# Kernel optimization log

Measured on AMD Instinct MI355X. Metric: run time of the kernel, lower is better.

## Reference

```python
import jax, jax.numpy as jnp
import numpy as np

B, S, D = 1, 2048, 1024
H, HD = 16, 64          # attention heads, head dim
DFF = 4096              # ffn hidden
IH, ID = 4, 64          # indexer heads / dim ('baseline' strategy)
TOP_K = 64
ROPE_BASE = 10000.0
LN_EPS = 1e-5


def setup_inputs() -> dict:
    key = jax.random.key(0)
    ks = jax.random.split(key, 12)
    g = lambda k, shape: (jax.random.normal(k, shape, dtype=jnp.float32) * 0.02)
    return {
        "x": jax.random.normal(ks[0], (B, S, D), dtype=jnp.float32),
        "w_qkv": g(ks[1], (D, 3 * D)),
        "w_o": g(ks[2], (D, D)),
        "ffn_w1": g(ks[3], (D, DFF)),
        "ffn_b1": jnp.zeros((DFF,), jnp.float32),
        "ffn_w2": g(ks[4], (DFF, D)),
        "ffn_b2": jnp.zeros((D,), jnp.float32),
        "ln1_g": jnp.ones((D,), jnp.float32),
        "ln1_b": jnp.zeros((D,), jnp.float32),
        "ln2_g": jnp.ones((D,), jnp.float32),
        "ln2_b": jnp.zeros((D,), jnp.float32),
        "idx_wq": g(ks[5], (D, IH * ID)),
        "idx_wk": g(ks[6], (D, ID)),
        "idx_ww": g(ks[7], (D, IH)),
    }


def _layernorm(x, g, b):
    m = jnp.mean(x, axis=-1, keepdims=True)
    v = jnp.var(x, axis=-1, keepdims=True)
    return (x - m) * jax.lax.rsqrt(v + LN_EPS) * g + b


def _rope(x):  # x: [B,S,H,HD], torchtune interleaved-pair convention
    half = HD // 2
    theta = 1.0 / (ROPE_BASE ** (jnp.arange(0, HD, 2, dtype=jnp.float32) / HD))  # [half]
    ang = jnp.arange(S, dtype=jnp.float32)[:, None] * theta                      # [S,half]
    cos = jnp.cos(ang)[None, :, None, :]
    sin = jnp.sin(ang)[None, :, None, :]
    xp = x.reshape(*x.shape[:-1], half, 2)
    x0, x1 = xp[..., 0], xp[..., 1]
    out = jnp.stack([x0 * cos - x1 * sin, x1 * cos + x0 * sin], axis=-1)
    return out.reshape(x.shape)


def reference(x, w_qkv, w_o, ffn_w1, ffn_b1, ffn_w2, ffn_b2,
              ln1_g, ln1_b, ln2_g, ln2_b, idx_wq, idx_wk, idx_ww):
    norm_x = _layernorm(x, ln1_g, ln1_b)

    qkv = norm_x @ w_qkv                              # [B,S,3D]
    q, k, v = jnp.split(qkv, 3, axis=-1)
    q = _rope(q.reshape(B, S, H, HD))
    k = _rope(k.reshape(B, S, H, HD))
    v = v.reshape(B, S, H, HD)

    # Lightning-style indexer: I[t,s] = sum_h w[t,h] * relu(q_i[t,h] . k_i[s])
    qi = (norm_x @ idx_wq).reshape(B, S, IH, ID)      # [B,S,IH,ID]
    ki = norm_x @ idx_wk                              # [B,S,ID]
    wi = norm_x @ idx_ww                              # [B,S,IH]
    qk = jnp.einsum("bthd,bsd->bths", qi, ki)         # [B,S,IH,S]
    index_scores = jnp.einsum("bth,bths->bts", wi, jax.nn.relu(qk))  # [B,S,S]

    # causal top-k token selection -> boolean mask
    causal = jnp.tril(jnp.ones((S, S), dtype=bool))
    masked_scores = jnp.where(causal, index_scores, -jnp.inf)
    _, topk_idx = jax.lax.top_k(masked_scores, TOP_K)  # [B,S,K]
    b_ix = jnp.arange(B)[:, None, None]
    q_ix = jnp.arange(S)[None, :, None]
    mask = jnp.zeros((B, S, S), dtype=bool).at[b_ix, q_ix, topk_idx].set(True)
    mask = mask & causal                               # [B,S,S]

    # masked SDPA
    logits = jnp.einsum("bqhd,bkhd->bhqk", q, k) / np.sqrt(HD)
    logits = jnp.where(mask[:, None, :, :], logits, -jnp.inf)
    attn = jax.nn.softmax(logits, axis=-1)
    attn_out = jnp.einsum("bhqk,bkhd->bqhd", attn, v).reshape(B, S, D)
    x = x + attn_out @ w_o

    h = _layernorm(x, ln2_g, ln2_b)
    ffn = jax.nn.gelu(h @ ffn_w1 + ffn_b1, approximate=False) @ ffn_w2 + ffn_b2
    return x + ffn
```

## Files before the change

kernel.cpp:

```cpp
#include <hip/hip_runtime.h>
#include <math.h>

#define S_LEN 2048
#define D_MODEL 1024
#define NHEAD 16
#define HDIM 64
#define DFF 4096
#define IH 4
#define IDM 64
#define TOPK 64
#define NIDX 336

typedef float f32x4 __attribute__((ext_vector_type(4)));
typedef short bf16x8 __attribute__((ext_vector_type(8)));

__device__ __forceinline__ unsigned short f2bf(float f) {
    unsigned u = __builtin_bit_cast(unsigned, f);
    u += 0x7fff + ((u >> 16) & 1);
    return (unsigned short)(u >> 16);
}
__device__ __forceinline__ float bf2f(unsigned short us) {
    return __builtin_bit_cast(float, (unsigned)us << 16);
}

__device__ __forceinline__ float gelu_exact(float v) {
    return 0.5f * v * (1.f + erff(v * 0.70710678118654752f));
}

__device__ __forceinline__ void gl_lds16(const void* g, void* l) {
    __builtin_amdgcn_global_load_lds(
        (const __attribute__((address_space(1))) void*)g,
        (__attribute__((address_space(3))) void*)l, 16, 0, 0);
}

__global__ __launch_bounds__(256) void ln_kernel(const float* __restrict__ x,
    const float* __restrict__ g, const float* __restrict__ b,
    float* __restrict__ outf, unsigned short* __restrict__ outb)
{
    int row = blockIdx.x, tid = threadIdx.x;
    const float4 v = *(const float4*)(x + (size_t)row * D_MODEL + tid * 4);
    float s = v.x + v.y + v.z + v.w;
    float ss = v.x * v.x + v.y * v.y + v.z * v.z + v.w * v.w;
    int lane = tid & 63, wv = tid >> 6;
    for (int o = 32; o; o >>= 1) { s += __shfl_xor(s, o); ss += __shfl_xor(ss, o); }
    __shared__ float rs[4], rss[4];
    if (lane == 0) { rs[wv] = s; rss[wv] = ss; }
    __syncthreads();
    float S = rs[0] + rs[1] + rs[2] + rs[3];
    float SS = rss[0] + rss[1] + rss[2] + rss[3];
    float mean = S * (1.f / D_MODEL);
    float var = SS * (1.f / D_MODEL) - mean * mean;
    float r = rsqrtf(var + 1e-5f);
    float4 gv = *(const float4*)(g + tid * 4);
    float4 bv = *(const float4*)(b + tid * 4);
    float4 o4;
    o4.x = (v.x - mean) * r * gv.x + bv.x;
    o4.y = (v.y - mean) * r * gv.y + bv.y;
    o4.z = (v.z - mean) * r * gv.z + bv.z;
    o4.w = (v.w - mean) * r * gv.w + bv.w;
    if (outf) *(float4*)(outf + (size_t)row * D_MODEL + tid * 4) = o4;
    if (outb) {
        ushort4 u4 = { f2bf(o4.x), f2bf(o4.y), f2bf(o4.z), f2bf(o4.w) };
        *(ushort4*)(outb + (size_t)row * D_MODEL + tid * 4) = u4;
    }
}

__global__ __launch_bounds__(256) void wtrans_kernel(const float* __restrict__ in,
    unsigned short* __restrict__ out, int K, int N)
{
    __shared__ float t[32][33];
    int k0 = blockIdx.y * 32, n0 = blockIdx.x * 32;
    int tid = threadIdx.x;
    int r = tid >> 5, c = tid & 31;
#pragma unroll
    for (int p = 0; p < 4; ++p)
        t[r + p * 8][c] = in[(size_t)(k0 + r + p * 8) * N + n0 + c];
    __syncthreads();
#pragma unroll
    for (int p = 0; p < 4; ++p)
        out[(size_t)(n0 + r + p * 8) * K + k0 + c] = f2bf(t[c][r + p * 8]);
}

__global__ __launch_bounds__(256) void wpack_kernel(const float* __restrict__ wq,
    const float* __restrict__ wk, const float* __restrict__ ww, float* __restrict__ Wc)
{
    int idx = blockIdx.x * 256 + threadIdx.x;
    if (idx >= D_MODEL * NIDX) return;
    int r = idx / NIDX, c = idx % NIDX;
    float v = 0.f;
    if (c < 256) v = wq[r * 256 + c];
    else if (c < 320) v = wk[r * 64 + (c - 256)];
    else if (c < 324) v = ww[r * 4 + (c - 320)];
    Wc[idx] = v;
}

__global__ __launch_bounds__(256) void gemm_bf16_n64(
    const unsigned short* __restrict__ A, const unsigned short* __restrict__ Bt,
    float* __restrict__ C, unsigned short* __restrict__ Cb,
    const float* __restrict__ bias, const float* __restrict__ R,
    int M, int N, int K, int act,
    float* __restrict__ P, int kchunk)
{
    __shared__ __attribute__((aligned(16))) unsigned short As[3][128 * 32];
    __shared__ __attribute__((aligned(16))) unsigned short Bs[3][64 * 32];
    int tid = threadIdx.x;
    int bm = blockIdx.y * 128, bn = blockIdx.x * 64;
    int wid = tid >> 6, lane = tid & 63;
    int wm = wid * 32;
    const unsigned short* Ab = A + (size_t)bm * K;
    const unsigned short* Bb = Bt + (size_t)bn * K;
    f32x4 acc[2][4];
#pragma unroll
    for (int i = 0; i < 2; ++i)
#pragma unroll
        for (int j = 0; j < 4; ++j)
            acc[i][j] = (f32x4){0.f, 0.f, 0.f, 0.f};

    int kbeg = blockIdx.z * kchunk;
    int NT = kchunk >> 5;
    int fr = lane & 15, fk = (lane >> 4) * 8;
    int e0 = tid * 8;
    int r0 = e0 >> 5, c0 = e0 & 31;

    auto STAGE = [&](int kt, int buf) {
        int k0 = kbeg + kt * 32;
        gl_lds16(Ab + (size_t)r0 * K + k0 + c0, &As[buf][e0]);
        gl_lds16(Ab + (size_t)(r0 + 64) * K + k0 + c0, &As[buf][e0 + 2048]);
        gl_lds16(Bb + (size_t)r0 * K + k0 + c0, &Bs[buf][e0]);
    };
    auto COMPUTE = [&](int buf) {
        bf16x8 af[2], bfv[4];
#pragma unroll
        for (int mi = 0; mi < 2; ++mi)
            af[mi] = *(const bf16x8*)&As[buf][(wm + mi * 16 + fr) * 32 + fk];
#pragma unroll
        for (int ni = 0; ni < 4; ++ni)
            bfv[ni] = *(const bf16x8*)&Bs[buf][(ni * 16 + fr) * 32 + fk];
#pragma unroll
        for (int mi = 0; mi < 2; ++mi)
#pragma unroll
            for (int ni = 0; ni < 4; ++ni)
                acc[mi][ni] = __builtin_amdgcn_mfma_f32_16x16x32_bf16(
                    af[mi], bfv[ni], acc[mi][ni], 0, 0, 0);
    };

    STAGE(0, 0);
    STAGE(1, 1);
    asm volatile("s_waitcnt vmcnt(3)" ::: "memory");
    __builtin_amdgcn_s_barrier();

    int kt = 0;
    for (; kt < NT - 2; ++kt) {
        STAGE(kt + 2, (kt + 2) % 3);
        COMPUTE(kt % 3);
        asm volatile("s_waitcnt vmcnt(3)" ::: "memory");
        __builtin_amdgcn_s_barrier();
    }
    COMPUTE((NT - 2) % 3);
    asm volatile("s_waitcnt vmcnt(0)" ::: "memory");
    __builtin_amdgcn_s_barrier();
    COMPUTE((NT - 1) % 3);

    int cl = lane & 15, rh = (lane >> 4) * 4;
    if (P) {
        float* Pz = P + (size_t)blockIdx.z * M * N;
#pragma unroll
        for (int mi = 0; mi < 2; ++mi)
#pragma unroll
            for (int ni = 0; ni < 4; ++ni) {
                int col = bn + ni * 16 + cl;
#pragma unroll
                for (int r = 0; r < 4; ++r) {
                    int row = bm + wm + mi * 16 + rh + r;
                    Pz[(size_t)row * N + col] = acc[mi][ni][r];
                }
            }
        return;
    }
#pragma unroll
    for (int mi = 0; mi < 2; ++mi) {
#pragma unroll
        for (int ni = 0; ni < 4; ++ni) {
            int col = bn + ni * 16 + cl;
            float bv = bias ? bias[col] : 0.f;
#pragma unroll
            for (int r = 0; r < 4; ++r) {
                int row = bm + wm + mi * 16 + rh + r;
                float v = acc[mi][ni][r] + bv;
                if (act) v = gelu_exact(v);
                size_t off = (size_t)row * N + col;
                if (R) v += R[off];
                if (C) C[off] = v;
                if (Cb) Cb[off] = f2bf(v);
            }
        }
    }
}

__global__ __launch_bounds__(256) void kreduce_kernel(const float* __restrict__ P,
    int nslice, float* __restrict__ C, const float* __restrict__ bias,
    const float* __restrict__ R, int M, int N)
{
    size_t total4 = (size_t)M * N / 4;
    size_t stride = (size_t)gridDim.x * 256;
    for (size_t i4 = blockIdx.x * 256 + threadIdx.x; i4 < total4; i4 += stride) {
        size_t off = i4 * 4;
        float4 v = *(const float4*)(P + off);
        for (int z = 1; z < nslice; ++z) {
            float4 p = *(const float4*)(P + (size_t)z * M * N + off);
            v.x += p.x; v.y += p.y; v.z += p.z; v.w += p.w;
        }
        if (bias) {
            float4 b4 = *(const float4*)(bias + (off % N));
            v.x += b4.x; v.y += b4.y; v.z += b4.z; v.w += b4.w;
        }
        if (R) {
            float4 r4 = *(const float4*)(R + off);
            v.x += r4.x; v.y += r4.y; v.z += r4.z; v.w += r4.w;
        }
        *(float4*)(C + off) = v;
    }
}

__global__ __launch_bounds__(256) void gemm64(const float* __restrict__ A,
    const float* __restrict__ B, float* __restrict__ C,
    int M, int N, int K,
    float* __restrict__ P, int kchunk)
{
    __shared__ float As[16][68];
    __shared__ float Bs[16][68];
    int tid = threadIdx.x;
    int bm = blockIdx.y, bn = blockIdx.x;
    int tx = tid & 15, ty = tid >> 4;
    int arow = tid >> 2;
    int acol = (tid & 3) << 2;
    int brow = tid >> 4;
    int bcol = (tid & 15) << 2;
    const float* Abase = A + (size_t)(bm * 64 + arow) * K + acol;
    float c[4][4] = {};
    int kbeg = blockIdx.z * kchunk;
    int kend = kbeg + kchunk;
    for (int k0 = kbeg; k0 < kend; k0 += 16) {
        float4 av = *(const float4*)(Abase + k0);
        As[acol + 0][arow] = av.x;
        As[acol + 1][arow] = av.y;
        As[acol + 2][arow] = av.z;
        As[acol + 3][arow] = av.w;
        int gcol = bn * 64 + bcol;
        const float* Bb = B + (size_t)(k0 + brow) * N;
        float4 bv;
        if (gcol + 3 < N) {
            bv = *(const float4*)(Bb + gcol);
        } else {
            bv.x = (gcol + 0 < N) ? Bb[gcol + 0] : 0.f;
            bv.y = (gcol + 1 < N) ? Bb[gcol + 1] : 0.f;
            bv.z = (gcol + 2 < N) ? Bb[gcol + 2] : 0.f;
            bv.w = (gcol + 3 < N) ? Bb[gcol + 3] : 0.f;
        }
        *(float4*)&Bs[brow][bcol] = bv;
        __syncthreads();
#pragma unroll
        for (int kk = 0; kk < 16; ++kk) {
            float4 a4 = *(const float4*)&As[kk][ty * 4];
            float4 b4 = *(const float4*)&Bs[kk][tx * 4];
            float av4[4] = { a4.x, a4.y, a4.z, a4.w };
            float bv4[4] = { b4.x, b4.y, b4.z, b4.w };
#pragma unroll
            for (int i = 0; i < 4; ++i)
#pragma unroll
                for (int j = 0; j < 4; ++j)
                    c[i][j] += av4[i] * bv4[j];
        }
        __syncthreads();
    }
    float* Out = P ? (P + (size_t)blockIdx.z * M * N) : C;
#pragma unroll
    for (int i = 0; i < 4; ++i) {
        int row = bm * 64 + ty * 4 + i;
#pragma unroll
        for (int j = 0; j < 4; ++j) {
            int col = bn * 64 + tx * 4 + j;
            if (col < N)
                Out[(size_t)row * N + col] = c[i][j];
        }
    }
}

__global__ __launch_bounds__(256) void rope_table_kernel(float* __restrict__ ct, float* __restrict__ st)
{
    int g = blockIdx.x * 256 + threadIdx.x;
    int t = g >> 5, i = g & 31;
    float theta = powf(10000.f, -(float)i / 32.f);
    float ang = (float)t * theta;
    ct[g] = cosf(ang);
    st[g] = sinf(ang);
}

__global__ __launch_bounds__(512) void rope_pack_kernel(
    const unsigned short* __restrict__ qkvb,
    const float* __restrict__ ct, const float* __restrict__ st,
    unsigned short* __restrict__ Qb, unsigned short* __restrict__ Kb,
    unsigned short* __restrict__ Vb)
{
    int t = blockIdx.x, tid = threadIdx.x;
    int h = tid >> 5, i = tid & 31;
    float c = ct[t * 32 + i], s = st[t * 32 + i];
    const unsigned short* base = qkvb + (size_t)t * (3 * D_MODEL);
    ushort2 q2 = *(const ushort2*)(base + h * HDIM + 2 * i);
    float q0 = bf2f(q2.x), q1 = bf2f(q2.y);
    ushort2 qo = { f2bf(q0 * c - q1 * s), f2bf(q1 * c + q0 * s) };
    *(ushort2*)(Qb + (size_t)t * D_MODEL + h * HDIM + 2 * i) = qo;
    ushort2 k2 = *(const ushort2*)(base + D_MODEL + h * HDIM + 2 * i);
    float k0 = bf2f(k2.x), k1 = bf2f(k2.y);
    ushort2 ko = { f2bf(k0 * c - k1 * s), f2bf(k1 * c + k0 * s) };
    *(ushort2*)(Kb + ((size_t)h * S_LEN + t) * HDIM + 2 * i) = ko;
    ushort2 v2 = *(const ushort2*)(base + 2 * D_MODEL + 2 * tid);
    int vh = tid >> 5, vd = (2 * tid) & 63;
    *(ushort2*)(Vb + ((size_t)vh * S_LEN + t) * HDIM + vd) = v2;
}

__global__ __launch_bounds__(256) void scores_kernel(const float* __restrict__ QIW,
    float* __restrict__ scores)
{
    int t0 = blockIdx.y * 64, s0 = blockIdx.x * 64;
    if (s0 > t0 + 63) return;
    __shared__ float qit[64][68];
    __shared__ float kit[64][68];
    __shared__ float wis[64][4];
    int tid = threadIdx.x;
    int tx = tid & 15, ty = tid >> 4;
    int lr = tid & 63;
    int cseg = tid >> 6;
    if (tid < 64) {
        float4 w4 = *(const float4*)(QIW + (size_t)(t0 + tid) * NIDX + 320);
        wis[tid][0] = w4.x; wis[tid][1] = w4.y; wis[tid][2] = w4.z; wis[tid][3] = w4.w;
    }
    float acc[4][4] = {};
#pragma unroll
    for (int h = 0; h < 4; ++h) {
        __syncthreads();
        const float* qrow = QIW + (size_t)(t0 + lr) * NIDX + h * 64 + cseg * 16;
        const float* krow = QIW + (size_t)(s0 + lr) * NIDX + 256 + cseg * 16;
#pragma unroll
        for (int q4 = 0; q4 < 4; ++q4) {
            int d = cseg * 16 + q4 * 4;
            float4 v = *(const float4*)(qrow + q4 * 4);
            qit[d + 0][lr] = v.x; qit[d + 1][lr] = v.y;
            qit[d + 2][lr] = v.z; qit[d + 3][lr] = v.w;
            if (h == 0) {
                float4 u = *(const float4*)(krow + q4 * 4);
                kit[d + 0][lr] = u.x; kit[d + 1][lr] = u.y;
                kit[d + 2][lr] = u.z; kit[d + 3][lr] = u.w;
            }
        }
        __syncthreads();
        float dot[4][4] = {};
#pragma unroll 8
        for (int d = 0; d < 64; ++d) {
            float4 a4 = *(const float4*)&qit[d][ty * 4];
            float4 b4 = *(const float4*)&kit[d][tx * 4];
            float av[4] = { a4.x, a4.y, a4.z, a4.w };
            float bv[4] = { b4.x, b4.y, b4.z, b4.w };
#pragma unroll
            for (int i = 0; i < 4; ++i)
#pragma unroll
                for (int j = 0; j < 4; ++j)
                    dot[i][j] += av[i] * bv[j];
        }
#pragma unroll
        for (int i = 0; i < 4; ++i) {
            float w = wis[ty * 4 + i][h];
#pragma unroll
            for (int j = 0; j < 4; ++j)
                acc[i][j] += w * fmaxf(dot[i][j], 0.f);
        }
    }
#pragma unroll
    for (int i = 0; i < 4; ++i) {
        float4 o4 = { acc[i][0], acc[i][1], acc[i][2], acc[i][3] };
        *(float4*)&scores[(size_t)(t0 + ty * 4 + i) * S_LEN + s0 + tx * 4] = o4;
    }
}

__global__ __launch_bounds__(256) void topk_kernel(const float* __restrict__ scores,
    int* __restrict__ topidx, int* __restrict__ topcnt)
{
    int t = blockIdx.x, tid = threadIdx.x;
    int n = t + 1;
    if (n <= TOPK) {
        if (tid < n) topidx[t * TOPK + tid] = tid;
        if (tid == 0) topcnt[t] = n;
        return;
    }
    __shared__ unsigned sc[S_LEN];
    __shared__ unsigned hist[256];
    __shared__ int selbin_s;
    __shared__ int cnt_out;
    __shared__ unsigned wsum[4];
    for (int j = tid; j < n; j += 256) {
        unsigned u = __builtin_bit_cast(unsigned, scores[(size_t)t * S_LEN + j]);
        sc[j] = (u & 0x80000000u) ? ~u : (u | 0x80000000u);
    }
    if (tid == 0) cnt_out = 0;
    int lane = tid & 63, wv = tid >> 6;
    unsigned prefix = 0;
    int kk = TOPK;
#pragma unroll
    for (int round = 0; round < 4; ++round) {
        int shift_pref = 32 - 8 * round;
        int shift_bin = 24 - 8 * round;
        hist[tid] = 0;
        __syncthreads();
        for (int j = tid; j < n; j += 256) {
            unsigned v = sc[j];
            if ((((unsigned long long)(v ^ prefix)) >> shift_pref) == 0)
                atomicAdd(&hist[(v >> shift_bin) & 0xff], 1u);
        }
        __syncthreads();
        if (wv == 0) {
            unsigned h0 = hist[4 * lane], h1 = hist[4 * lane + 1];
            unsigned h2 = hist[4 * lane + 2], h3 = hist[4 * lane + 3];
            unsigned s3 = h3, s2 = h2 + s3, s1 = h1 + s2, s0 = h0 + s1;
            unsigned acc = s0;
            for (int off = 1; off < 64; off <<= 1) {
                unsigned o = __shfl_down(acc, off);
                if (lane + off < 64) acc += o;
            }
            unsigned above = acc - s0;
            hist[4 * lane]     = s0 + above;
            hist[4 * lane + 1] = s1 + above;
            hist[4 * lane + 2] = s2 + above;
            hist[4 * lane + 3] = s3 + above;
        }
        __syncthreads();
        {
            unsigned sufb = hist[tid];
            unsigned sufn = (tid < 255) ? hist[tid + 1] : 0u;
            if (sufb >= (unsigned)kk && sufn < (unsigned)kk)
                selbin_s = tid;
        }
        __syncthreads();
        int b = selbin_s;
        unsigned above = (b < 255) ? hist[b + 1] : 0u;
        kk -= (int)above;
        prefix |= ((unsigned)b) << shift_bin;
        __syncthreads();
    }
    unsigned T = prefix;
    int chunk = (n + 255) >> 8;
    int jb = tid * chunk;
    int je = jb + chunk; if (je > n) je = n;
    int ties = 0;
    for (int j = jb; j < je; ++j) {
        unsigned v = sc[j];
        if (v > T) { int o = atomicAdd(&cnt_out, 1); topidx[t * TOPK + o] = j; }
        else if (v == T) ++ties;
    }
    unsigned inc = (unsigned)ties;
    for (int off = 1; off < 64; off <<= 1) {
        unsigned o = __shfl_up(inc, off);
        if (lane >= off) inc += o;
    }
    if (lane == 63) wsum[wv] = inc;
    __syncthreads();
    unsigned woff = 0;
    for (int w = 0; w < wv; ++w) woff += wsum[w];
    int rank = (int)(woff + inc) - ties;
    for (int j = jb; j < je && rank < kk; ++j) {
        if (sc[j] == T) {
            int o = atomicAdd(&cnt_out, 1);
            topidx[t * TOPK + o] = j;
            ++rank;
        }
    }
    if (tid == 0) topcnt[t] = TOPK;
}

__global__ __launch_bounds__(256) void attn_kernel(
    const unsigned short* __restrict__ Qb, const unsigned short* __restrict__ Kb,
    const unsigned short* __restrict__ Vb,
    const int* __restrict__ topidx, const int* __restrict__ topcnt,
    unsigned short* __restrict__ out)
{
    int t = blockIdx.x, tid = threadIdx.x;
    __shared__ int sel[TOPK];
    if (tid < TOPK) sel[tid] = topidx[t * TOPK + tid];
    __syncthreads();
    int cnt = topcnt[t];
    int lane = tid & 63, wv = tid >> 6;
    int h = blockIdx.y * 4 + wv;
    int klo = lane >> 3, oct = lane & 7;
    int rows[8];
    bool valid[8];
#pragma unroll
    for (int kg = 0; kg < 8; ++kg) {
        int k = kg * 8 + klo;
        valid[kg] = (k < cnt);
        rows[kg] = sel[valid[kg] ? k : 0];
    }
    bf16x8 q8 = *(const bf16x8*)(Qb + (size_t)t * D_MODEL + h * HDIM + oct * 8);
    float qf[8];
#pragma unroll
    for (int e = 0; e < 8; ++e) qf[e] = bf2f((unsigned short)q8[e]);

    const unsigned short* kbase = Kb + (size_t)h * S_LEN * HDIM + oct * 8;
    float p[8];
#pragma unroll
    for (int kg = 0; kg < 8; ++kg) {
        bf16x8 k8 = *(const bf16x8*)(kbase + (size_t)rows[kg] * HDIM);
        float d = 0.f;
#pragma unroll
        for (int e = 0; e < 8; ++e)
            d += bf2f((unsigned short)k8[e]) * qf[e];
        d += __shfl_xor(d, 1);
        d += __shfl_xor(d, 2);
        d += __shfl_xor(d, 4);
        p[kg] = valid[kg] ? d * 0.125f : -INFINITY;
    }
    float m = p[0];
#pragma unroll
    for (int kg = 1; kg < 8; ++kg) m = fmaxf(m, p[kg]);
    m = fmaxf(m, __shfl_xor(m, 8));
    m = fmaxf(m, __shfl_xor(m, 16));
    m = fmaxf(m, __shfl_xor(m, 32));
    float sum = 0.f;
#pragma unroll
    for (int kg = 0; kg < 8; ++kg) { p[kg] = __expf(p[kg] - m); sum += p[kg]; }
    sum += __shfl_xor(sum, 8);
    sum += __shfl_xor(sum, 16);
    sum += __shfl_xor(sum, 32);
    float rs = 1.f / sum;
    const unsigned short* vbase = Vb + (size_t)h * S_LEN * HDIM + oct * 8;
    float facc[8] = {};
#pragma unroll
    for (int kg = 0; kg < 8; ++kg) {
        bf16x8 v8 = *(const bf16x8*)(vbase + (size_t)rows[kg] * HDIM);
        float pw = p[kg] * rs;
#pragma unroll
        for (int e = 0; e < 8; ++e)
            facc[e] += pw * bf2f((unsigned short)v8[e]);
    }
#pragma unroll
    for (int e = 0; e < 8; ++e) {
        facc[e] += __shfl_xor(facc[e], 8);
        facc[e] += __shfl_xor(facc[e], 16);
        facc[e] += __shfl_xor(facc[e], 32);
    }
    if (klo == 0) {
        ushort4 o0 = { f2bf(facc[0]), f2bf(facc[1]), f2bf(facc[2]), f2bf(facc[3]) };
        ushort4 o1 = { f2bf(facc[4]), f2bf(facc[5]), f2bf(facc[6]), f2bf(facc[7]) };
        *(ushort4*)(out + (size_t)t * D_MODEL + h * HDIM + oct * 8) = o0;
        *(ushort4*)(out + (size_t)t * D_MODEL + h * HDIM + oct * 8 + 4) = o1;
    }
}

extern "C" void kernel_launch(void* const* d_in, const int* in_sizes, int n_in,
                              void* d_out, int out_size, void* d_ws, size_t ws_size,
                              hipStream_t stream)
{
    const float* x      = (const float*)d_in[0];
    const float* w_qkv  = (const float*)d_in[1];
    const float* w_o    = (const float*)d_in[2];
    const float* ffn_w1 = (const float*)d_in[3];
    const float* ffn_b1 = (const float*)d_in[4];
    const float* ffn_w2 = (const float*)d_in[5];
    const float* ffn_b2 = (const float*)d_in[6];
    const float* ln1_g  = (const float*)d_in[7];
    const float* ln1_b  = (const float*)d_in[8];
    const float* ln2_g  = (const float*)d_in[9];
    const float* ln2_b  = (const float*)d_in[10];
    const float* idx_wq = (const float*)d_in[11];
    const float* idx_wk = (const float*)d_in[12];
    const float* idx_ww = (const float*)d_in[13];
    float* outp = (float*)d_out;

    const size_t MB = 1ull << 20;
    char* ws = (char*)d_ws;
    float*          normx    = (float*)(ws + 0);
    unsigned short* attno_bf = (unsigned short*)(ws + 0);
    float*          Pf2      = (float*)(ws + 0);
    unsigned short* normx_bf = (unsigned short*)(ws + 8 * MB);
    unsigned short* h2_bf    = normx_bf;
    unsigned short* qkv_bf   = (unsigned short*)(ws + 12 * MB);
    int*            topidx   = (int*)(ws + 12 * MB);
    int*            topcnt   = (int*)(ws + 12 * MB + 512 * 1024);
    unsigned short* wqkv_t   = (unsigned short*)(ws + 24 * MB);
    unsigned short* wo_t     = (unsigned short*)(ws + 30 * MB);
    unsigned short* w1_t     = (unsigned short*)(ws + 32 * MB);
    unsigned short* w2_t     = (unsigned short*)(ws + 40 * MB);
    unsigned short* Qb       = (unsigned short*)(ws + 48 * MB);
    unsigned short* Kb       = (unsigned short*)(ws + 52 * MB);
    unsigned short* Vb       = (unsigned short*)(ws + 56 * MB);
    float*          ctab     = (float*)(ws + 60 * MB);
    float*          stab     = (float*)(ws + 60 * MB + 256 * 1024);
    float*          P_idx    = (float*)(ws + 60 * MB);
    float*          scoresb  = (float*)(ws + 60 * MB);
    float*          Pwo      = (float*)(ws + 60 * MB);
    unsigned short* ffn1_bf  = (unsigned short*)(ws + 60 * MB);
    float*          QIW      = (float*)(ws + 76 * MB);
    float*          Wc       = (float*)(ws + 79 * MB);

    dim3 blk256(256);
    auto g64n = [](int N, int M) { return dim3(N / 64, M / 128); };

    ln_kernel<<<S_LEN, blk256, 0, stream>>>(x, ln1_g, ln1_b, normx, normx_bf);
    rope_table_kernel<<<(S_LEN * 32) / 256, blk256, 0, stream>>>(ctab, stab);
    wtrans_kernel<<<dim3(3 * D_MODEL / 32, D_MODEL / 32), blk256, 0, stream>>>(w_qkv, wqkv_t, D_MODEL, 3 * D_MODEL);
    wtrans_kernel<<<dim3(D_MODEL / 32, D_MODEL / 32), blk256, 0, stream>>>(w_o, wo_t, D_MODEL, D_MODEL);
    wtrans_kernel<<<dim3(DFF / 32, D_MODEL / 32), blk256, 0, stream>>>(ffn_w1, w1_t, D_MODEL, DFF);
    wtrans_kernel<<<dim3(D_MODEL / 32, DFF / 32), blk256, 0, stream>>>(ffn_w2, w2_t, DFF, D_MODEL);
    wpack_kernel<<<(D_MODEL * NIDX + 255) / 256, blk256, 0, stream>>>(idx_wq, idx_wk, idx_ww, Wc);
    gemm_bf16_n64<<<g64n(3 * D_MODEL, S_LEN), blk256, 0, stream>>>(normx_bf, wqkv_t,
        nullptr, qkv_bf, nullptr, nullptr, S_LEN, 3 * D_MODEL, D_MODEL, 0, nullptr, D_MODEL);
    rope_pack_kernel<<<S_LEN, dim3(512), 0, stream>>>(qkv_bf, ctab, stab, Qb, Kb, Vb);
    gemm64<<<dim3((NIDX + 63) / 64, S_LEN / 64, 4), blk256, 0, stream>>>(normx, Wc,
        nullptr, S_LEN, NIDX, D_MODEL, P_idx, D_MODEL / 4);
    kreduce_kernel<<<1024, blk256, 0, stream>>>(P_idx, 4, QIW, nullptr, nullptr, S_LEN, NIDX);
    scores_kernel<<<dim3(32, 32), blk256, 0, stream>>>(QIW, scoresb);
    topk_kernel<<<S_LEN, blk256, 0, stream>>>(scoresb, topidx, topcnt);
    attn_kernel<<<dim3(S_LEN, 4), blk256, 0, stream>>>(Qb, Kb, Vb, topidx, topcnt, attno_bf);
    gemm_bf16_n64<<<dim3(D_MODEL / 64, S_LEN / 128, 2), blk256, 0, stream>>>(attno_bf, wo_t,
        nullptr, nullptr, nullptr, nullptr, S_LEN, D_MODEL, D_MODEL, 0, Pwo, D_MODEL / 2);
    kreduce_kernel<<<1024, blk256, 0, stream>>>(Pwo, 2, outp, nullptr, x, S_LEN, D_MODEL);
    ln_kernel<<<S_LEN, blk256, 0, stream>>>(outp, ln2_g, ln2_b, nullptr, h2_bf);
    gemm_bf16_n64<<<g64n(DFF, S_LEN), blk256, 0, stream>>>(h2_bf, w1_t,
        nullptr, ffn1_bf, ffn_b1, nullptr, S_LEN, DFF, D_MODEL, 1, nullptr, D_MODEL);
    gemm_bf16_n64<<<dim3(D_MODEL / 64, S_LEN / 128, 4), blk256, 0, stream>>>(ffn1_bf, w2_t,
        nullptr, nullptr, nullptr, nullptr, S_LEN, D_MODEL, DFF, 0, Pf2, DFF / 4);
    kreduce_kernel<<<1024, blk256, 0, stream>>>(Pf2, 4, outp, ffn_b2, outp, S_LEN, D_MODEL);
}
```

Baseline: 273.9 us.

## Merge weight-prep launches and load GEMM A fragments directly into registers

Six small preprocessing launches (rope table, four weight transposes, indexer weight pack) become one prep_kernel that dispatches on block index, cutting launch overhead. The bf16 GEMM stops staging A tiles through LDS: each wave loads its A fragments straight from global memory into registers one k-step ahead, and only B still goes through the triple-buffered LDS pipeline. MFMA sections are wrapped in s_setprio raises. Uncoalesced per-lane global A loads and the changed vmcnt accounting may add latency or stalls in exchange for less LDS traffic and smaller shared memory.

```diff
diff --git a/kernel.cpp b/kernel.cpp
--- a/kernel.cpp
+++ b/kernel.cpp
@@ -65,12 +65,11 @@
     }
 }
 
-__global__ __launch_bounds__(256) void wtrans_kernel(const float* __restrict__ in,
-    unsigned short* __restrict__ out, int K, int N)
+__device__ __forceinline__ void wtrans_body(const float* __restrict__ in,
+    unsigned short* __restrict__ out, int K, int N, int bx, int by, int tid)
 {
     __shared__ float t[32][33];
-    int k0 = blockIdx.y * 32, n0 = blockIdx.x * 32;
-    int tid = threadIdx.x;
+    int k0 = by * 32, n0 = bx * 32;
     int r = tid >> 5, c = tid & 31;
 #pragma unroll
     for (int p = 0; p < 4; ++p)
@@ -81,17 +80,50 @@
         out[(size_t)(n0 + r + p * 8) * K + k0 + c] = f2bf(t[c][r + p * 8]);
 }
 
-__global__ __launch_bounds__(256) void wpack_kernel(const float* __restrict__ wq,
-    const float* __restrict__ wk, const float* __restrict__ ww, float* __restrict__ Wc)
-{
-    int idx = blockIdx.x * 256 + threadIdx.x;
-    if (idx >= D_MODEL * NIDX) return;
-    int r = idx / NIDX, c = idx % NIDX;
-    float v = 0.f;
-    if (c < 256) v = wq[r * 256 + c];
-    else if (c < 320) v = wk[r * 64 + (c - 256)];
-    else if (c < 324) v = ww[r * 4 + (c - 320)];
-    Wc[idx] = v;
+#define PREP_ROPE   256
+#define PREP_WQKV   3072
+#define PREP_WO     1024
+#define PREP_W1     4096
+#define PREP_W2     4096
+#define PREP_WPACK  1344
+#define PREP_TOTAL  (PREP_ROPE + PREP_WQKV + PREP_WO + PREP_W1 + PREP_W2 + PREP_WPACK)
+__global__ __launch_bounds__(256) void prep_kernel(
+    const float* __restrict__ w_qkv, const float* __restrict__ w_o,
+    const float* __restrict__ w1, const float* __restrict__ w2,
+    const float* __restrict__ wq, const float* __restrict__ wk, const float* __restrict__ ww,
+    unsigned short* __restrict__ wqkv_t, unsigned short* __restrict__ wo_t,
+    unsigned short* __restrict__ w1_t, unsigned short* __restrict__ w2_t,
+    float* __restrict__ Wc, float* __restrict__ ct, float* __restrict__ st)
+{
+    int b = blockIdx.x, tid = threadIdx.x;
+    if (b < PREP_ROPE) {
+        int g = b * 256 + tid;
+        int t = g >> 5, i = g & 31;
+        float theta = powf(10000.f, -(float)i / 32.f);
+        float ang = (float)t * theta;
+        ct[g] = cosf(ang);
+        st[g] = sinf(ang);
+        return;
+    }
+    b -= PREP_ROPE;
+    if (b < PREP_WQKV) { wtrans_body(w_qkv, wqkv_t, 1024, 3072, b % 96, b / 96, tid); return; }
+    b -= PREP_WQKV;
+    if (b < PREP_WO)   { wtrans_body(w_o, wo_t, 1024, 1024, b % 32, b / 32, tid); return; }
+    b -= PREP_WO;
+    if (b < PREP_W1)   { wtrans_body(w1, w1_t, 1024, 4096, b % 128, b / 128, tid); return; }
+    b -= PREP_W1;
+    if (b < PREP_W2)   { wtrans_body(w2, w2_t, 4096, 1024, b % 32, b / 32, tid); return; }
+    b -= PREP_W2;
+    {
+        int idx = b * 256 + tid;
+        if (idx >= D_MODEL * NIDX) return;
+        int r = idx / NIDX, c = idx % NIDX;
+        float v = 0.f;
+        if (c < 256) v = wq[r * 256 + c];
+        else if (c < 320) v = wk[r * 64 + (c - 256)];
+        else if (c < 324) v = ww[r * 4 + (c - 320)];
+        Wc[idx] = v;
+    }
 }
 
 __global__ __launch_bounds__(256) void gemm_bf16_n64(
@@ -101,7 +133,6 @@
     int M, int N, int K, int act,
     float* __restrict__ P, int kchunk)
 {
-    __shared__ __attribute__((aligned(16))) unsigned short As[3][128 * 32];
     __shared__ __attribute__((aligned(16))) unsigned short Bs[3][64 * 32];
     int tid = threadIdx.x;
     int bm = blockIdx.y * 128, bn = blockIdx.x * 64;
@@ -121,45 +152,53 @@
     int fr = lane & 15, fk = (lane >> 4) * 8;
     int e0 = tid * 8;
     int r0 = e0 >> 5, c0 = e0 & 31;
-
-    auto STAGE = [&](int kt, int buf) {
-        int k0 = kbeg + kt * 32;
-        gl_lds16(Ab + (size_t)r0 * K + k0 + c0, &As[buf][e0]);
-        gl_lds16(Ab + (size_t)(r0 + 64) * K + k0 + c0, &As[buf][e0 + 2048]);
-        gl_lds16(Bb + (size_t)r0 * K + k0 + c0, &Bs[buf][e0]);
+    const unsigned short* Ar0 = Ab + (size_t)(wm + fr) * K + fk;
+    const unsigned short* Ar1 = Ab + (size_t)(wm + 16 + fr) * K + fk;
+
+    auto STAGE_B = [&](int kt, int buf) {
+        gl_lds16(Bb + (size_t)r0 * K + kbeg + kt * 32 + c0, &Bs[buf][e0]);
     };
-    auto COMPUTE = [&](int buf) {
-        bf16x8 af[2], bfv[4];
-#pragma unroll
-        for (int mi = 0; mi < 2; ++mi)
-            af[mi] = *(const bf16x8*)&As[buf][(wm + mi * 16 + fr) * 32 + fk];
+    auto COMPUTE = [&](int buf, bf16x8 a0, bf16x8 a1) {
+        bf16x8 bfv[4];
 #pragma unroll
         for (int ni = 0; ni < 4; ++ni)
             bfv[ni] = *(const bf16x8*)&Bs[buf][(ni * 16 + fr) * 32 + fk];
-#pragma unroll
-        for (int mi = 0; mi < 2; ++mi)
-#pragma unroll
-            for (int ni = 0; ni < 4; ++ni)
-                acc[mi][ni] = __builtin_amdgcn_mfma_f32_16x16x32_bf16(
-                    af[mi], bfv[ni], acc[mi][ni], 0, 0, 0);
+        __builtin_amdgcn_s_setprio(1);
+#pragma unroll
+        for (int ni = 0; ni < 4; ++ni) {
+            acc[0][ni] = __builtin_amdgcn_mfma_f32_16x16x32_bf16(a0, bfv[ni], acc[0][ni], 0, 0, 0);
+            acc[1][ni] = __builtin_amdgcn_mfma_f32_16x16x32_bf16(a1, bfv[ni], acc[1][ni], 0, 0, 0);
+        }
+        __builtin_amdgcn_s_setprio(0);
     };
 
-    STAGE(0, 0);
-    STAGE(1, 1);
+    STAGE_B(0, 0);
+    STAGE_B(1, 1);
+    bf16x8 a0 = *(const bf16x8*)(Ar0 + kbeg);
+    bf16x8 a1 = *(const bf16x8*)(Ar1 + kbeg);
     asm volatile("s_waitcnt vmcnt(3)" ::: "memory");
     __builtin_amdgcn_s_barrier();
 
-    int kt = 0;
-    for (; kt < NT - 2; ++kt) {
-        STAGE(kt + 2, (kt + 2) % 3);
-        COMPUTE(kt % 3);
+    for (int kt = 0; kt < NT - 2; ++kt) {
+        STAGE_B(kt + 2, (kt + 2) % 3);
+        int kn = kbeg + (kt + 1) * 32;
+        bf16x8 an0 = *(const bf16x8*)(Ar0 + kn);
+        bf16x8 an1 = *(const bf16x8*)(Ar1 + kn);
+        COMPUTE(kt % 3, a0, a1);
+        a0 = an0; a1 = an1;
         asm volatile("s_waitcnt vmcnt(3)" ::: "memory");
         __builtin_amdgcn_s_barrier();
     }
-    COMPUTE((NT - 2) % 3);
-    asm volatile("s_waitcnt vmcnt(0)" ::: "memory");
-    __builtin_amdgcn_s_barrier();
-    COMPUTE((NT - 1) % 3);
+    {
+        int kn = kbeg + (NT - 1) * 32;
+        bf16x8 an0 = *(const bf16x8*)(Ar0 + kn);
+        bf16x8 an1 = *(const bf16x8*)(Ar1 + kn);
+        COMPUTE((NT - 2) % 3, a0, a1);
+        a0 = an0; a1 = an1;
+        asm volatile("s_waitcnt vmcnt(2)" ::: "memory");
+        __builtin_amdgcn_s_barrier();
+        COMPUTE((NT - 1) % 3, a0, a1);
+    }
 
     int cl = lane & 15, rh = (lane >> 4) * 4;
     if (P) {
@@ -286,16 +325,6 @@
     }
 }
 
-__global__ __launch_bounds__(256) void rope_table_kernel(float* __restrict__ ct, float* __restrict__ st)
-{
-    int g = blockIdx.x * 256 + threadIdx.x;
-    int t = g >> 5, i = g & 31;
-    float theta = powf(10000.f, -(float)i / 32.f);
-    float ang = (float)t * theta;
-    ct[g] = cosf(ang);
-    st[g] = sinf(ang);
-}
-
 __global__ __launch_bounds__(512) void rope_pack_kernel(
     const unsigned short* __restrict__ qkvb,
     const float* __restrict__ ct, const float* __restrict__ st,
@@ -604,12 +633,8 @@
     auto g64n = [](int N, int M) { return dim3(N / 64, M / 128); };
 
     ln_kernel<<<S_LEN, blk256, 0, stream>>>(x, ln1_g, ln1_b, normx, normx_bf);
-    rope_table_kernel<<<(S_LEN * 32) / 256, blk256, 0, stream>>>(ctab, stab);
-    wtrans_kernel<<<dim3(3 * D_MODEL / 32, D_MODEL / 32), blk256, 0, stream>>>(w_qkv, wqkv_t, D_MODEL, 3 * D_MODEL);
-    wtrans_kernel<<<dim3(D_MODEL / 32, D_MODEL / 32), blk256, 0, stream>>>(w_o, wo_t, D_MODEL, D_MODEL);
-    wtrans_kernel<<<dim3(DFF / 32, D_MODEL / 32), blk256, 0, stream>>>(ffn_w1, w1_t, D_MODEL, DFF);
-    wtrans_kernel<<<dim3(D_MODEL / 32, DFF / 32), blk256, 0, stream>>>(ffn_w2, w2_t, DFF, D_MODEL);
-    wpack_kernel<<<(D_MODEL * NIDX + 255) / 256, blk256, 0, stream>>>(idx_wq, idx_wk, idx_ww, Wc);
+    prep_kernel<<<PREP_TOTAL, blk256, 0, stream>>>(w_qkv, w_o, ffn_w1, ffn_w2,
+        idx_wq, idx_wk, idx_ww, wqkv_t, wo_t, w1_t, w2_t, Wc, ctab, stab);
     gemm_bf16_n64<<<g64n(3 * D_MODEL, S_LEN), blk256, 0, stream>>>(normx_bf, wqkv_t,
         nullptr, qkv_bf, nullptr, nullptr, S_LEN, 3 * D_MODEL, D_MODEL, 0, nullptr, D_MODEL);
     rope_pack_kernel<<<S_LEN, dim3(512), 0, stream>>>(qkv_bf, ctab, stab, Qb, Kb, Vb);
```

Measured after the change: 282.4 us. 3.1% more time.
